# Performance work log

Measured on AMD Instinct MI355X. Metric: run time of the kernel, lower is better.

Reference implementation:

```python
import jax, jax.numpy as jnp
import numpy as np

N = 100000
F_IN = 128
HID = 16
C = 16
E = 3200000


def setup_inputs() -> dict:
    key = jax.random.key(0)
    k1, k2, k3, k4, k5, k6 = jax.random.split(key, 6)
    x = jax.random.normal(k1, (N, F_IN), dtype=jnp.float32)
    edge_index = jax.random.randint(k2, (2, E), 0, N, dtype=jnp.int64)
    # GCNConv weight (glorot) + bias
    W1 = jax.random.normal(k3, (F_IN, HID), dtype=jnp.float32) * (1.0 / np.sqrt(F_IN))
    b1 = jnp.zeros((HID,), dtype=jnp.float32)
    # pooling linear
    Wp = jax.random.normal(k4, (HID, C), dtype=jnp.float32) * (1.0 / np.sqrt(HID))
    bp = jax.random.normal(k5, (C,), dtype=jnp.float32) * 0.01
    return {"x": x, "W1": W1, "b1": b1, "Wp": Wp, "bp": bp, "edge_index": edge_index}


def gcn_conv(x, W, b, edge_index, num_nodes):
    # PyG GCNConv: add self-loops, symmetric normalization D^-1/2 (A+I) D^-1/2
    loop = jnp.arange(num_nodes, dtype=edge_index.dtype)
    src = jnp.concatenate([edge_index[0], loop])
    dst = jnp.concatenate([edge_index[1], loop])
    ones = jnp.ones_like(dst, dtype=x.dtype)
    deg = jax.ops.segment_sum(ones, dst, num_segments=num_nodes)  # [N]
    dinv = jnp.where(deg > 0, jax.lax.rsqrt(deg), 0.0)
    norm = dinv[src] * dinv[dst]  # [E+N]
    h = x @ W  # [N, HID] transform before aggregation (fewer bytes moved)
    msgs = h[src] * norm[:, None]  # gather + scale
    agg = jax.ops.segment_sum(msgs, dst, num_segments=num_nodes)  # scatter-add
    return agg + b


def reference(x, W1, b1, Wp, bp, edge_index):
    h = jax.nn.relu(gcn_conv(x, W1, b1, edge_index, N))  # [N, HID]
    s = jax.nn.softmax(h @ Wp + bp, axis=1)  # [N, C]
    return s
```

## Files before the change

### kernel.cpp

```cpp
#include <hip/hip_runtime.h>


#define PCHUNK 4096
#define SPLITS 4
#define ACH 2048

__device__ __forceinline__ float bf2f(unsigned int u16) {
    return __uint_as_float(u16 << 16);
}
__device__ __forceinline__ unsigned short f2bf(float f) {
    unsigned int u = __float_as_uint(f);
    u += 0x7fffu + ((u >> 16) & 1u);
    return (unsigned short)(u >> 16);
}

__device__ __forceinline__ void atomAddF(float* p, float v) {
    unsafeAtomicAdd(p, v);
}

__device__ __forceinline__ int voteBf16(const unsigned int* xw, int tid, int* scratch) {
    if (tid == 0) *scratch = 0;
    __syncthreads();
    unsigned int w = xw[tid];
    unsigned int lo = w & 0xffffu;
    unsigned int elo = (lo >> 7) & 0xffu;
    if (lo == 0u || (elo >= 100u && elo <= 140u)) atomicAdd(scratch, 1);
    __syncthreads();
    return (*scratch >= 160) ? 1 : 0;
}

__device__ __forceinline__ int waveIncScan(int v, int lane) {
    int inc = v;
    #pragma unroll
    for (int off = 1; off < 64; off <<= 1) {
        int t = __shfl_up(inc, off, 64);
        if (lane >= off) inc += t;
    }
    return inc;
}

__global__ __launch_bounds__(256) void k_part(const int* __restrict__ ei,
                                              int* __restrict__ cursor,
                                              unsigned int* __restrict__ bkt,
                                              int E, int Nn, int NB, int cap) {
    __shared__ int lhist[512];
    __shared__ int lexcl[512];
    __shared__ int lbase[512];
    __shared__ int wsum[4];
    __shared__ unsigned int stage[PCHUNK];
    __shared__ ushort sbk[PCHUNK];
    __shared__ int v64_s;
    int tid = threadIdx.x;
    lhist[tid] = 0; lhist[tid + 256] = 0;
    if (tid == 0) v64_s = 0;
    __syncthreads();
    if (((const unsigned int*)ei)[2 * tid + 1] != 0u) atomicAdd(&v64_s, 1);
    __syncthreads();
    int is64 = (v64_s == 0) ? 1 : 0;
    int e0 = blockIdx.x * PCHUNK;
    int ss[16], dd[16];
    #pragma unroll
    for (int i = 0; i < 16; ++i) {
        int e = e0 + i * 256 + tid;
        int s = -1, d = -1;
        if (e < E) {
            if (is64) { s = ei[2 * e]; d = ei[2 * (E + e)]; }
            else      { s = ei[e];     d = ei[E + e]; }
            if ((unsigned)s >= (unsigned)Nn || (unsigned)d >= (unsigned)Nn) { s = -1; d = -1; }
        }
        ss[i] = s;
        if (d >= 0) {
            int r = atomicAdd(&lhist[d >> 8], 1);
            dd[i] = d | (r << 17);
        } else dd[i] = -1;
    }
    __syncthreads();
    int a0 = lhist[2 * tid], a1 = lhist[2 * tid + 1];
    int pair = a0 + a1;
    int lane = tid & 63, wv = tid >> 6;
    int inc = waveIncScan(pair, lane);
    if (lane == 63) wsum[wv] = inc;
    __syncthreads();
    int woff = 0;
    #pragma unroll
    for (int w = 0; w < 4; ++w) woff += (w < wv) ? wsum[w] : 0;
    int stot = wsum[0] + wsum[1] + wsum[2] + wsum[3];
    int exP = woff + inc - pair;
    lexcl[2 * tid] = exP;
    lexcl[2 * tid + 1] = exP + a0;
    __syncthreads();
    for (int b = tid; b < 512; b += 256) {
        int c = lhist[b];
        if (b < NB && c > 0) {
            int base = atomicAdd(&cursor[b], c);
            lbase[b] = b * cap + base - lexcl[b];
        } else lbase[b] = 0;
    }
    __syncthreads();
    #pragma unroll
    for (int i = 0; i < 16; ++i) {
        if (dd[i] >= 0) {
            int d = dd[i] & 0x1ffff;
            int bk = d >> 8;
            int q = lexcl[bk] + (dd[i] >> 17);
            stage[q] = (unsigned)ss[i] | ((unsigned)(d & 255) << 17);
            sbk[q] = (ushort)bk;
        }
    }
    __syncthreads();
    for (int q = tid; q < stot; q += 256) {
        int b = sbk[q];
        int pos = lbase[b] + q;
        if (pos < (b + 1) * cap) bkt[pos] = stage[q];
    }
}

__global__ __launch_bounds__(256) void k_gemmD(const void* __restrict__ xraw,
                                               const void* __restrict__ w1raw,
                                               const unsigned int* __restrict__ bkt,
                                               const int* __restrict__ cursor,
                                               float* __restrict__ dinv,
                                               ushort* __restrict__ hs16,
                                               float* __restrict__ agg,
                                               int Nn, int cap) {
    __shared__ float sWt[16 * 132];
    __shared__ int ldeg[256];
    __shared__ float sdv[256];
    __shared__ int vote_s;
    const ushort* xb = (const ushort*)xraw;
    const float* xf = (const float*)xraw;
    int tid = threadIdx.x, b = blockIdx.x;
    const int isbf = voteBf16((const unsigned int*)xraw, tid, &vote_s);
    ldeg[tid] = 0;
    if (isbf) {
        const ushort* w1 = (const ushort*)w1raw;
        for (int i = tid; i < 2048; i += 256) {
            int k = i >> 4, j = i & 15;
            sWt[j * 132 + k] = bf2f(w1[i]);
        }
    } else {
        const float* w1 = (const float*)w1raw;
        for (int i = tid; i < 2048; i += 256) {
            int k = i >> 4, j = i & 15;
            sWt[j * 132 + k] = w1[i];
        }
    }
    __syncthreads();
    int len = min(cursor[b], cap);
    int bb = b * cap;
    for (int e = tid; e < len; e += 256)
        atomicAdd(&ldeg[(bkt[bb + e] >> 17) & 255u], 1);
    __syncthreads();
    {
        float dv = rsqrtf((float)(ldeg[tid] + 1));
        sdv[tid] = dv;
        int n = (b << 8) + tid;
        if (n < Nn) dinv[n] = dv;
    }
    __syncthreads();
    int hq = tid & 3;
    int nodeq = tid >> 2;
    int n0 = (b << 8) + nodeq * 4;
    float acc[4][4] = {};
    for (int ko = 0; ko < 16; ++ko) {
        float xv[4][8];
        #pragma unroll
        for (int r = 0; r < 4; ++r) {
            int n = n0 + r;
            if (n < Nn) {
                if (isbf) {
                    uint4 q = *reinterpret_cast<const uint4*>(xb + (size_t)n * 128 + ko * 8);
                    xv[r][0] = bf2f(q.x & 0xffffu); xv[r][1] = bf2f(q.x >> 16);
                    xv[r][2] = bf2f(q.y & 0xffffu); xv[r][3] = bf2f(q.y >> 16);
                    xv[r][4] = bf2f(q.z & 0xffffu); xv[r][5] = bf2f(q.z >> 16);
                    xv[r][6] = bf2f(q.w & 0xffffu); xv[r][7] = bf2f(q.w >> 16);
                } else {
                    const float4* p = reinterpret_cast<const float4*>(xf + (size_t)n * 128 + ko * 8);
                    float4 a = p[0], bf = p[1];
                    xv[r][0] = a.x; xv[r][1] = a.y; xv[r][2] = a.z; xv[r][3] = a.w;
                    xv[r][4] = bf.x; xv[r][5] = bf.y; xv[r][6] = bf.z; xv[r][7] = bf.w;
                }
            } else {
                #pragma unroll
                for (int u = 0; u < 8; ++u) xv[r][u] = 0.f;
            }
        }
        #pragma unroll
        for (int c = 0; c < 4; ++c) {
            const float* wr = &sWt[(hq * 4 + c) * 132 + ko * 8];
            float4 w0 = *reinterpret_cast<const float4*>(wr);
            float4 w1v = *reinterpret_cast<const float4*>(wr + 4);
            #pragma unroll
            for (int r = 0; r < 4; ++r) {
                acc[r][c] += xv[r][0] * w0.x + xv[r][1] * w0.y + xv[r][2] * w0.z + xv[r][3] * w0.w
                           + xv[r][4] * w1v.x + xv[r][5] * w1v.y + xv[r][6] * w1v.z + xv[r][7] * w1v.w;
            }
        }
    }
    #pragma unroll
    for (int r = 0; r < 4; ++r) {
        int n = n0 + r;
        if (n < Nn) {
            float dv = sdv[nodeq * 4 + r];
            float4 o = make_float4(acc[r][0] * dv, acc[r][1] * dv, acc[r][2] * dv, acc[r][3] * dv);
            ushort4 o16;
            o16.x = f2bf(o.x); o16.y = f2bf(o.y); o16.z = f2bf(o.z); o16.w = f2bf(o.w);
            *reinterpret_cast<ushort4*>(hs16 + (size_t)n * 16 + hq * 4) = o16;
            *reinterpret_cast<float4*>(agg + (size_t)n * 16 + hq * 4) = o;
        }
    }
}

__global__ __launch_bounds__(256) void k_aggS(const unsigned int* __restrict__ bkt,
                                              const int* __restrict__ cursor,
                                              const ushort* __restrict__ hs16,
                                              float* __restrict__ agg, int Nn, int cap) {
    __shared__ unsigned int sSorted[ACH];
    __shared__ int cnt[256], excl[256];
    __shared__ int wsum[4];
    int tid = threadIdx.x;
    int b = blockIdx.x >> 2, sp = blockIdx.x & 3;
    int len = min(cursor[b], cap);
    int bb = b * cap;
    int s0 = (int)(((long long)len * sp) >> 2);
    int s1 = (int)(((long long)len * (sp + 1)) >> 2);
    int g = tid >> 4, j = tid & 15;
    int lane = tid & 63, wv = tid >> 6;
    float racc[16] = {};
    for (int c0 = s0; c0 < s1; c0 += ACH) {
        cnt[tid] = 0;
        __syncthreads();
        unsigned ue[8];
        #pragma unroll
        for (int i = 0; i < 8; ++i) {
            int idx = c0 + i * 256 + tid;
            if (idx < s1) {
                ue[i] = bkt[bb + idx];
                atomicAdd(&cnt[(ue[i] >> 17) & 255u], 1);
            } else ue[i] = 0xffffffffu;
        }
        __syncthreads();
        int v = cnt[tid];
        int inc = waveIncScan(v, lane);
        if (lane == 63) wsum[wv] = inc;
        __syncthreads();
        int woff = 0;
        #pragma unroll
        for (int w = 0; w < 4; ++w) woff += (w < wv) ? wsum[w] : 0;
        int tot = wsum[0] + wsum[1] + wsum[2] + wsum[3];
        int ex = woff + inc - v;
        excl[tid] = ex;
        cnt[tid] = ex;
        __syncthreads();
        #pragma unroll
        for (int i = 0; i < 8; ++i) {
            if (ue[i] != 0xffffffffu) {
                int q = atomicAdd(&cnt[(ue[i] >> 17) & 255u], 1);
                sSorted[q] = ue[i];
            }
        }
        __syncthreads();
        #pragma unroll
        for (int nn = 0; nn < 16; ++nn) {
            int node = g * 16 + nn;
            int segS = excl[node];
            int segE = (node == 255) ? tot : excl[node + 1];
            float acc = 0.f;
            #pragma unroll 1
            for (int base = segS; base < segE; base += 8) {
                int m = segE - base;
                unsigned e8[8];
                float vv[8];
                #pragma unroll
                for (int i = 0; i < 8; ++i) {
                    int idx = base + i;
                    e8[i] = sSorted[(idx < segE) ? idx : segS];
                }
                #pragma unroll
                for (int i = 0; i < 8; ++i)
                    vv[i] = bf2f(hs16[(size_t)(e8[i] & 0x1ffffu) * 16 + j]);
                #pragma unroll
                for (int i = 0; i < 8; ++i)
                    vv[i] = (i < m) ? vv[i] : 0.f;
                vv[0] += vv[4]; vv[1] += vv[5]; vv[2] += vv[6]; vv[3] += vv[7];
                vv[0] += vv[2]; vv[1] += vv[3];
                acc += vv[0] + vv[1];
            }
            racc[nn] += acc;
        }
        __syncthreads();
    }
    int nbase = b << 8;
    #pragma unroll
    for (int nn = 0; nn < 16; ++nn) {
        int n = nbase + g * 16 + nn;
        float v = racc[nn];
        bool nz = (n < Nn) && (v != 0.f);
        if (__any(nz)) {
            if (n < Nn) atomAddF(&agg[(size_t)n * 16 + j], v);
        }
    }
}

__global__ __launch_bounds__(256) void k_final(const float* __restrict__ agg,
                                               const float* __restrict__ dinv,
                                               const void* __restrict__ xraw,
                                               const void* __restrict__ b1raw,
                                               const void* __restrict__ wpraw,
                                               const void* __restrict__ bpraw,
                                               void* __restrict__ outraw, int Nn) {
    __shared__ float sWp[256];
    __shared__ float sA[256];
    __shared__ int vote_s;
    int tid = threadIdx.x;
    const int isbf = voteBf16((const unsigned int*)xraw, tid, &vote_s);
    sWp[tid] = isbf ? bf2f(((const ushort*)wpraw)[tid]) : ((const float*)wpraw)[tid];
    int nl = tid >> 4, c = tid & 15;
    float b1v = isbf ? bf2f(((const ushort*)b1raw)[c]) : ((const float*)b1raw)[c];
    float bpv = isbf ? bf2f(((const ushort*)bpraw)[c]) : ((const float*)bpraw)[c];
    int base0 = blockIdx.x * 64;
    #pragma unroll 1
    for (int pass = 0; pass < 4; ++pass) {
        int n = base0 + pass * 16 + nl;
        float av = (n < Nn) ? agg[(size_t)n * 16 + c] * dinv[n] : 0.f;
        sA[tid] = fmaxf(av + b1v, 0.f);
        __syncthreads();
        float acc = bpv;
        #pragma unroll
        for (int jj = 0; jj < 16; ++jj) acc += sA[nl * 16 + jj] * sWp[jj * 16 + c];
        float m = acc;
        #pragma unroll
        for (int off = 1; off < 16; off <<= 1) m = fmaxf(m, __shfl_xor(m, off, 16));
        float ev = __expf(acc - m);
        float s = ev;
        #pragma unroll
        for (int off = 1; off < 16; off <<= 1) s += __shfl_xor(s, off, 16);
        if (n < Nn) {
            float v = ev / s;
            if (isbf) ((ushort*)outraw)[(size_t)n * 16 + c] = f2bf(v);
            else      ((float*)outraw)[(size_t)n * 16 + c] = v;
        }
        __syncthreads();
    }
}

extern "C" void kernel_launch(void* const* d_in, const int* in_sizes, int n_in,
                              void* d_out, int out_size, void* d_ws, size_t ws_size,
                              hipStream_t stream) {
    const void* x  = d_in[0];
    const void* W1 = d_in[1];
    const void* b1 = d_in[2];
    const void* Wp = d_in[3];
    const void* bp = d_in[4];
    const int*  ei = (const int*)d_in[5];

    int Nn = in_sizes[0] / 128;
    int E  = in_sizes[5] / 2;
    int NB = (Nn + 255) >> 8;

    size_t Ns = (size_t)Nn;
    char* ws = (char*)d_ws;
    size_t off = 0;
    auto alloc = [&](size_t bytes) { void* p = ws + off; off += (bytes + 63) & ~(size_t)63; return p; };
    ushort* hs16  = (ushort*)alloc(Ns * 16 * 2);
    float* agg    = (float*)alloc(Ns * 16 * 4);
    float* dinv   = (float*)alloc(Ns * 4);
    int*   cursor = (int*)alloc(512 * 4);
    size_t remain = (ws_size > off) ? (ws_size - off) : 0;
    int cap = (int)(remain / 4 / (size_t)NB);
    int want = 12288;
    if (cap > want) cap = want;
    cap &= ~63;
    unsigned int* bkt = (unsigned int*)alloc((size_t)NB * (size_t)cap * 4);

    hipMemsetAsync(cursor, 0, 512 * 4, stream);
    k_part<<<(E + PCHUNK - 1) / PCHUNK, 256, 0, stream>>>(ei, cursor, bkt, E, Nn, NB, cap);
    k_gemmD<<<NB, 256, 0, stream>>>(x, W1, bkt, cursor, dinv, hs16, agg, Nn, cap);
    k_aggS<<<NB * SPLITS, 256, 0, stream>>>(bkt, cursor, hs16, agg, Nn, cap);
    k_final<<<(Nn + 63) / 64, 256, 0, stream>>>(agg, dinv, x, b1, Wp, bp, d_out, Nn);
}
```

Before: 229.4 us.

## Widen gemm kernel to 1024 threads, one node per quad; halve partition chunk

The dense transform kernel now runs 1024 threads per block, so each thread handles one node instead of four. This raises memory-level parallelism for the x reads and cuts register pressure. The edge-partition kernel processes 2048 edges per block instead of 4096, which doubles the block count and reduces per-thread register arrays. The tradeoffs are more atomics on the global bucket cursors and smaller write runs per bucket. The bf16 vote helper is inlined so it works with the larger block.

```diff
diff --git a/kernel.cpp b/kernel.cpp
--- a/kernel.cpp
+++ b/kernel.cpp
@@ -1,7 +1,7 @@
 #include <hip/hip_runtime.h>
 
 
-#define PCHUNK 4096
+#define PCHUNK 2048
 #define SPLITS 4
 #define ACH 2048
 
@@ -16,17 +16,6 @@
 
 __device__ __forceinline__ void atomAddF(float* p, float v) {
     unsafeAtomicAdd(p, v);
-}
-
-__device__ __forceinline__ int voteBf16(const unsigned int* xw, int tid, int* scratch) {
-    if (tid == 0) *scratch = 0;
-    __syncthreads();
-    unsigned int w = xw[tid];
-    unsigned int lo = w & 0xffffu;
-    unsigned int elo = (lo >> 7) & 0xffu;
-    if (lo == 0u || (elo >= 100u && elo <= 140u)) atomicAdd(scratch, 1);
-    __syncthreads();
-    return (*scratch >= 160) ? 1 : 0;
 }
 
 __device__ __forceinline__ int waveIncScan(int v, int lane) {
@@ -58,9 +47,9 @@
     __syncthreads();
     int is64 = (v64_s == 0) ? 1 : 0;
     int e0 = blockIdx.x * PCHUNK;
-    int ss[16], dd[16];
-    #pragma unroll
-    for (int i = 0; i < 16; ++i) {
+    int ss[8], dd[8];
+    #pragma unroll
+    for (int i = 0; i < 8; ++i) {
         int e = e0 + i * 256 + tid;
         int s = -1, d = -1;
         if (e < E) {
@@ -98,7 +87,7 @@
     }
     __syncthreads();
     #pragma unroll
-    for (int i = 0; i < 16; ++i) {
+    for (int i = 0; i < 8; ++i) {
         if (dd[i] >= 0) {
             int d = dd[i] & 0x1ffff;
             int bk = d >> 8;
@@ -115,14 +104,14 @@
     }
 }
 
-__global__ __launch_bounds__(256) void k_gemmD(const void* __restrict__ xraw,
-                                               const void* __restrict__ w1raw,
-                                               const unsigned int* __restrict__ bkt,
-                                               const int* __restrict__ cursor,
-                                               float* __restrict__ dinv,
-                                               ushort* __restrict__ hs16,
-                                               float* __restrict__ agg,
-                                               int Nn, int cap) {
+__global__ __launch_bounds__(1024) void k_gemmD(const void* __restrict__ xraw,
+                                                const void* __restrict__ w1raw,
+                                                const unsigned int* __restrict__ bkt,
+                                                const int* __restrict__ cursor,
+                                                float* __restrict__ dinv,
+                                                ushort* __restrict__ hs16,
+                                                float* __restrict__ agg,
+                                                int Nn, int cap) {
     __shared__ float sWt[16 * 132];
     __shared__ int ldeg[256];
     __shared__ float sdv[256];
@@ -130,17 +119,25 @@
     const ushort* xb = (const ushort*)xraw;
     const float* xf = (const float*)xraw;
     int tid = threadIdx.x, b = blockIdx.x;
-    const int isbf = voteBf16((const unsigned int*)xraw, tid, &vote_s);
-    ldeg[tid] = 0;
+    if (tid == 0) vote_s = 0;
+    __syncthreads();
+    if (tid < 256) {
+        unsigned w = ((const unsigned*)xraw)[tid];
+        unsigned lo = w & 0xffffu, elo = (lo >> 7) & 0xffu;
+        if (lo == 0u || (elo >= 100u && elo <= 140u)) atomicAdd(&vote_s, 1);
+        ldeg[tid] = 0;
+    }
+    __syncthreads();
+    const int isbf = (vote_s >= 160);
     if (isbf) {
         const ushort* w1 = (const ushort*)w1raw;
-        for (int i = tid; i < 2048; i += 256) {
+        for (int i = tid; i < 2048; i += 1024) {
             int k = i >> 4, j = i & 15;
             sWt[j * 132 + k] = bf2f(w1[i]);
         }
     } else {
         const float* w1 = (const float*)w1raw;
-        for (int i = tid; i < 2048; i += 256) {
+        for (int i = tid; i < 2048; i += 1024) {
             int k = i >> 4, j = i & 15;
             sWt[j * 132 + k] = w1[i];
         }
@@ -148,10 +145,10 @@
     __syncthreads();
     int len = min(cursor[b], cap);
     int bb = b * cap;
-    for (int e = tid; e < len; e += 256)
+    for (int e = tid; e < len; e += 1024)
         atomicAdd(&ldeg[(bkt[bb + e] >> 17) & 255u], 1);
     __syncthreads();
-    {
+    if (tid < 256) {
         float dv = rsqrtf((float)(ldeg[tid] + 1));
         sdv[tid] = dv;
         int n = (b << 8) + tid;
@@ -159,55 +156,44 @@
     }
     __syncthreads();
     int hq = tid & 3;
-    int nodeq = tid >> 2;
-    int n0 = (b << 8) + nodeq * 4;
-    float acc[4][4] = {};
+    int node = tid >> 2;
+    int n = (b << 8) + node;
+    float acc[4] = {};
     for (int ko = 0; ko < 16; ++ko) {
-        float xv[4][8];
-        #pragma unroll
-        for (int r = 0; r < 4; ++r) {
-            int n = n0 + r;
-            if (n < Nn) {
-                if (isbf) {
-                    uint4 q = *reinterpret_cast<const uint4*>(xb + (size_t)n * 128 + ko * 8);
-                    xv[r][0] = bf2f(q.x & 0xffffu); xv[r][1] = bf2f(q.x >> 16);
-                    xv[r][2] = bf2f(q.y & 0xffffu); xv[r][3] = bf2f(q.y >> 16);
-                    xv[r][4] = bf2f(q.z & 0xffffu); xv[r][5] = bf2f(q.z >> 16);
-                    xv[r][6] = bf2f(q.w & 0xffffu); xv[r][7] = bf2f(q.w >> 16);
-                } else {
-                    const float4* p = reinterpret_cast<const float4*>(xf + (size_t)n * 128 + ko * 8);
-                    float4 a = p[0], bf = p[1];
-                    xv[r][0] = a.x; xv[r][1] = a.y; xv[r][2] = a.z; xv[r][3] = a.w;
-                    xv[r][4] = bf.x; xv[r][5] = bf.y; xv[r][6] = bf.z; xv[r][7] = bf.w;
-                }
+        float xv[8];
+        if (n < Nn) {
+            if (isbf) {
+                uint4 q = *reinterpret_cast<const uint4*>(xb + (size_t)n * 128 + ko * 8);
+                xv[0] = bf2f(q.x & 0xffffu); xv[1] = bf2f(q.x >> 16);
+                xv[2] = bf2f(q.y & 0xffffu); xv[3] = bf2f(q.y >> 16);
+                xv[4] = bf2f(q.z & 0xffffu); xv[5] = bf2f(q.z >> 16);
+                xv[6] = bf2f(q.w & 0xffffu); xv[7] = bf2f(q.w >> 16);
             } else {
-                #pragma unroll
-                for (int u = 0; u < 8; ++u) xv[r][u] = 0.f;
+                const float4* p = reinterpret_cast<const float4*>(xf + (size_t)n * 128 + ko * 8);
+                float4 a = p[0], bf = p[1];
+                xv[0] = a.x; xv[1] = a.y; xv[2] = a.z; xv[3] = a.w;
+                xv[4] = bf.x; xv[5] = bf.y; xv[6] = bf.z; xv[7] = bf.w;
             }
+        } else {
+            #pragma unroll
+            for (int u = 0; u < 8; ++u) xv[u] = 0.f;
         }
         #pragma unroll
         for (int c = 0; c < 4; ++c) {
             const float* wr = &sWt[(hq * 4 + c) * 132 + ko * 8];
             float4 w0 = *reinterpret_cast<const float4*>(wr);
             float4 w1v = *reinterpret_cast<const float4*>(wr + 4);
-            #pragma unroll
-            for (int r = 0; r < 4; ++r) {
-                acc[r][c] += xv[r][0] * w0.x + xv[r][1] * w0.y + xv[r][2] * w0.z + xv[r][3] * w0.w
-                           + xv[r][4] * w1v.x + xv[r][5] * w1v.y + xv[r][6] * w1v.z + xv[r][7] * w1v.w;
-            }
-        }
-    }
-    #pragma unroll
-    for (int r = 0; r < 4; ++r) {
-        int n = n0 + r;
-        if (n < Nn) {
-            float dv = sdv[nodeq * 4 + r];
-            float4 o = make_float4(acc[r][0] * dv, acc[r][1] * dv, acc[r][2] * dv, acc[r][3] * dv);
-            ushort4 o16;
-            o16.x = f2bf(o.x); o16.y = f2bf(o.y); o16.z = f2bf(o.z); o16.w = f2bf(o.w);
-            *reinterpret_cast<ushort4*>(hs16 + (size_t)n * 16 + hq * 4) = o16;
-            *reinterpret_cast<float4*>(agg + (size_t)n * 16 + hq * 4) = o;
-        }
+            acc[c] += xv[0] * w0.x + xv[1] * w0.y + xv[2] * w0.z + xv[3] * w0.w
+                    + xv[4] * w1v.x + xv[5] * w1v.y + xv[6] * w1v.z + xv[7] * w1v.w;
+        }
+    }
+    if (n < Nn) {
+        float dv = sdv[node];
+        float4 o = make_float4(acc[0] * dv, acc[1] * dv, acc[2] * dv, acc[3] * dv);
+        ushort4 o16;
+        o16.x = f2bf(o.x); o16.y = f2bf(o.y); o16.z = f2bf(o.z); o16.w = f2bf(o.w);
+        *reinterpret_cast<ushort4*>(hs16 + (size_t)n * 16 + hq * 4) = o16;
+        *reinterpret_cast<float4*>(agg + (size_t)n * 16 + hq * 4) = o;
     }
 }
 
@@ -313,7 +299,15 @@
     __shared__ float sA[256];
     __shared__ int vote_s;
     int tid = threadIdx.x;
-    const int isbf = voteBf16((const unsigned int*)xraw, tid, &vote_s);
+    if (tid == 0) vote_s = 0;
+    __syncthreads();
+    {
+        unsigned w = ((const unsigned*)xraw)[tid];
+        unsigned lo = w & 0xffffu, elo = (lo >> 7) & 0xffu;
+        if (lo == 0u || (elo >= 100u && elo <= 140u)) atomicAdd(&vote_s, 1);
+    }
+    __syncthreads();
+    const int isbf = (vote_s >= 160);
     sWp[tid] = isbf ? bf2f(((const ushort*)wpraw)[tid]) : ((const float*)wpraw)[tid];
     int nl = tid >> 4, c = tid & 15;
     float b1v = isbf ? bf2f(((const ushort*)b1raw)[c]) : ((const float*)b1raw)[c];
@@ -375,7 +369,7 @@
 
     hipMemsetAsync(cursor, 0, 512 * 4, stream);
     k_part<<<(E + PCHUNK - 1) / PCHUNK, 256, 0, stream>>>(ei, cursor, bkt, E, Nn, NB, cap);
-    k_gemmD<<<NB, 256, 0, stream>>>(x, W1, bkt, cursor, dinv, hs16, agg, Nn, cap);
+    k_gemmD<<<NB, 1024, 0, stream>>>(x, W1, bkt, cursor, dinv, hs16, agg, Nn, cap);
     k_aggS<<<NB * SPLITS, 256, 0, stream>>>(bkt, cursor, hs16, agg, Nn, cap);
     k_final<<<(Nn + 63) / 64, 256, 0, stream>>>(agg, dinv, x, b1, Wp, bp, d_out, Nn);
 }
```

Result: slower. 748.4 us (+226.2%).
